# Kernel optimization log

Measured on AMD Instinct MI355X. Metric: run time of the kernel, lower is better.

The kernel has to match this reference:

```python
import jax, jax.numpy as jnp
import numpy as np
from jax import lax

ROWS, COLS, HID = 5, 5, 4
N = ROWS * COLS
NUM_NEURONS = 128


def _nbr_indices(i, direction):
    # Faithful to get_neighbor_hidden, including the row-wrap behavior of
    # 'col-1'/'col+1' (no column bounds check in the original code).
    row, col = divmod(i, COLS)
    up = (row - 1) * COLS + col
    dn = (row + 1) * COLS + col
    lf = row * COLS + col - 1
    rt = row * COLS + col + 1
    return [up, dn, lf, rt] if direction == 'f' else [up, dn, rt, lf]


def _gather_neighbors(h, idxs):
    # h: (N, bs, HID); returns (bs, 4) of the 4th hidden feature per neighbor
    bs = h.shape[1]
    cols_list = [h[j][:, 3] if 0 <= j < N else jnp.zeros((bs,), h.dtype) for j in idxs]
    return jnp.stack(cols_list, axis=1)


def _make_step(Wx, Wh, Wn, b, direction):
    # One timestep: nodes updated sequentially (node i sees already-updated
    # up/left neighbors within the same timestep, matching the torch loop).
    def step(carry, x_t):  # x_t: (N, bs)
        h, c = carry  # each (N, bs, HID)
        for i in range(N):
            nb = _gather_neighbors(h, _nbr_indices(i, direction))  # (bs,4)
            gates = x_t[i][:, None] @ Wx + h[i] @ Wh + nb @ Wn + b  # (bs,4H)
            ig, fg, og, cc = jnp.split(gates, 4, axis=1)
            nc = jax.nn.sigmoid(fg) * c[i] + jax.nn.sigmoid(ig) * jnp.tanh(cc)
            nh = jax.nn.sigmoid(og) * jnp.tanh(nc)
            h = h.at[i].set(nh)
            c = c.at[i].set(nc)
        return (h, c), None
    return step


def _forward(x, h0f, c0f, h0b, c0b, Wx_f, Wh_f, Wn_f, b_f,
             Wx_b, Wh_b, Wn_b, b_b, W_ff, b_ff, W_out, b_out):
    bs = x.shape[0]
    x_seq = jnp.transpose(x, (2, 1, 0))  # (T, N, bs)
    (hf, cf), _ = lax.scan(_make_step(Wx_f, Wh_f, Wn_f, b_f, 'f'), (h0f, c0f), x_seq)
    (hb, cb), _ = lax.scan(_make_step(Wx_b, Wh_b, Wn_b, b_b, 'b'), (h0b, c0b), x_seq[::-1])
    H_fwd = jnp.transpose(hf, (1, 0, 2))  # (bs, N, HID)
    H_bwd = jnp.transpose(hb, (1, 0, 2))
    H = jnp.concatenate([H_fwd, H_bwd], axis=2).reshape(bs, -1)  # (bs, 200)
    ff = jax.nn.sigmoid(H @ W_ff + b_ff)
    return jax.nn.softmax(ff @ W_out + b_out, axis=1)


def setup_inputs() -> dict:
    key = jax.random.key(0)
    ks = jax.random.split(key, 16)
    bs, T = 8192, 128
    d = {}
    d['x'] = jax.random.normal(ks[0], (bs, N, T), jnp.float32)
    for nm, k in zip(['h0f', 'c0f', 'h0b', 'c0b'], ks[1:5]):
        d[nm] = jax.random.normal(k, (N, bs, HID), jnp.float32) * 0.01
    def lin(k, i, o):
        return jax.random.normal(k, (i, o), jnp.float32) * (1.0 / np.sqrt(i))
    d['Wx_f'] = lin(ks[5], 1, 4 * HID)
    d['Wh_f'] = lin(ks[6], HID, 4 * HID)
    d['Wn_f'] = lin(ks[7], 4, 4 * HID)
    d['b_f'] = jnp.zeros((4 * HID,), jnp.float32)
    d['Wx_b'] = lin(ks[8], 1, 4 * HID)
    d['Wh_b'] = lin(ks[9], HID, 4 * HID)
    d['Wn_b'] = lin(ks[10], 4, 4 * HID)
    d['b_b'] = jnp.zeros((4 * HID,), jnp.float32)
    d['W_ff'] = lin(ks[11], N * 2 * HID, NUM_NEURONS)
    d['b_ff'] = jnp.zeros((NUM_NEURONS,), jnp.float32)
    d['W_out'] = lin(ks[12], NUM_NEURONS, 2)
    d['b_out'] = jnp.zeros((2,), jnp.float32)
    return d


def reference(x, h0f, c0f, h0b, c0b, Wx_f, Wh_f, Wn_f, b_f,
              Wx_b, Wh_b, Wn_b, b_b, W_ff, b_ff, W_out, b_out):
    return _forward(x, h0f, c0f, h0b, c0b, Wx_f, Wh_f, Wn_f, b_f,
                    Wx_b, Wh_b, Wn_b, b_b, W_ff, b_ff, W_out, b_out)
```

## Files before the change

kernel.cpp:

```cpp
#include <hip/hip_runtime.h>
#include <stddef.h>

#define BS 8192
#define NNODE 25
#define TT 128
#define TCH 16
#define NW (TT / TCH)
#define XPAD 65
#define LOG2E 1.4426950408889634f

typedef float v2f __attribute__((ext_vector_type(2)));
typedef float v4f __attribute__((ext_vector_type(4)));

__device__ __forceinline__ float ex2(float x) { return __builtin_amdgcn_exp2f(x); }
__device__ __forceinline__ float rcp_(float x) { return __builtin_amdgcn_rcpf(x); }

__device__ float g_hf[NNODE * BS * 4];
__device__ float g_hb[NNODE * BS * 4];

template <int K>
__device__ __forceinline__ float bcast4(float v) {
  int s = __builtin_bit_cast(int, v);
  int r = __builtin_amdgcn_update_dpp(0, s, (K * 0x55), 0xF, 0xF, true);
  return __builtin_bit_cast(float, r);
}

__device__ __forceinline__ void acc2(v2f& A, v2f& B, float s, v2f wa, v2f wb) {
  v2f sv = {s, s};
  A = __builtin_elementwise_fma(sv, wa, A);
  B = __builtin_elementwise_fma(sv, wb, B);
}

template <int DIR>
__device__ __forceinline__ void rnn_run(
    int tid, const float* __restrict__ xblk, float* __restrict__ xs,
    const float* __restrict__ h0, const float* __restrict__ c0,
    const float* __restrict__ Wx, const float* __restrict__ Wh,
    const float* __restrict__ Wn, const float* __restrict__ Bb,
    float* __restrict__ ho, int b) {
  const int d = tid & 3;
  const int bl = tid >> 2;
  const int cI = d, cF = 4 + d, cO = 8 + d, cC = 12 + d;
  const float sS = -LOG2E, sC = 2.0f * LOG2E;

  v2f wA[9], wB[9];
  wA[0] = v2f{sS * Wx[cI], sS * Wx[cF]};
  wB[0] = v2f{sS * Wx[cO], sC * Wx[cC]};
#pragma unroll
  for (int k = 0; k < 4; ++k) {
    wA[1 + k] = v2f{sS * Wh[k * 16 + cI], sS * Wh[k * 16 + cF]};
    wB[1 + k] = v2f{sS * Wh[k * 16 + cO], sC * Wh[k * 16 + cC]};
  }
  const int nrow[4] = {0, 1, DIR ? 3 : 2, DIR ? 2 : 3};
#pragma unroll
  for (int k = 0; k < 4; ++k) {
    wA[5 + k] = v2f{sS * Wn[nrow[k] * 16 + cI], sS * Wn[nrow[k] * 16 + cF]};
    wB[5 + k] = v2f{sS * Wn[nrow[k] * 16 + cO], sC * Wn[nrow[k] * 16 + cC]};
  }
  const v2f bA = {sS * Bb[cI], sS * Bb[cF]};
  const v2f bB = {sS * Bb[cO], sC * Bb[cC]};

  float h[NNODE], c[NNODE], b3[NNODE];
#pragma unroll
  for (int i = 0; i < NNODE; ++i) {
    h[i] = h0[(i * BS + b) * 4 + d];
    c[i] = c0[(i * BS + b) * 4 + d];
    b3[i] = bcast4<3>(h[i]);
  }

  const int t4 = tid & 3;
  const int s0 = tid >> 2;

  for (int w = 0; w < NW; ++w) {
    __syncthreads();
#pragma unroll
    for (int r = 0; r < NNODE; ++r) {
      const int seg = s0 + 64 * r;
      const int sbl = seg / 25;
      const int sii = seg - sbl * 25;
      const int tb = (DIR ? (TT - TCH - TCH * w) : (TCH * w)) + 4 * t4;
      const v4f v = *(const v4f*)(xblk + ((size_t)sbl * NNODE + sii) * TT + tb);
#pragma unroll
      for (int j = 0; j < 4; ++j) {
        const int kk = DIR ? (15 - 4 * t4 - j) : (4 * t4 + j);
        xs[(kk * NNODE + sii) * XPAD + sbl] = v[j];
      }
    }
    __syncthreads();

#pragma unroll 1
    for (int kk = 0; kk < TCH; ++kk) {
      float xq[NNODE];
#pragma unroll
      for (int i = 0; i < NNODE; ++i) xq[i] = xs[(kk * NNODE + i) * XPAD + bl];

#pragma unroll
      for (int r = 0; r < 5; ++r) {
        v2f PA[5], PB[5];
#pragma unroll
        for (int j = 0; j < 5; ++j) {
          const int i = r * 5 + j;
          const float f0 = bcast4<0>(h[i]);
          const float f1 = bcast4<1>(h[i]);
          const float f2 = bcast4<2>(h[i]);
          v2f A = bA, B = bB;
          acc2(A, B, xq[i], wA[0], wB[0]);
          acc2(A, B, f0, wA[1], wB[1]);
          acc2(A, B, f1, wA[2], wB[2]);
          acc2(A, B, f2, wA[3], wB[3]);
          acc2(A, B, b3[i], wA[4], wB[4]);
          if (i >= 5) acc2(A, B, b3[i - 5], wA[5], wB[5]);
          if (i < 20) acc2(A, B, b3[i + 5], wA[6], wB[6]);
          if (i < 24) acc2(A, B, b3[i + 1], wA[8], wB[8]);
          PA[j] = A;
          PB[j] = B;
        }

#pragma unroll
        for (int j = 0; j < 5; ++j) {
          const int i = r * 5 + j;
          v2f A = PA[j], B = PB[j];
          if (i >= 1) acc2(A, B, b3[i - 1], wA[7], wB[7]);

          const float Ei = ex2(A.x);
          const float Ef = ex2(A.y);
          const float Eo = ex2(B.x);
          const float Ec = ex2(B.y);
          const v2f Dif = v2f{Ei, Ef} + v2f{1.0f, 1.0f};
          const v2f Ecpm = v2f{Ec, Ec} + v2f{1.0f, -1.0f};
          const float P = Dif.x * Ecpm.x;
          const float num = fmaf(c[i], P, Ecpm.y * Dif.y);
          const float nc = num * rcp_(Dif.y * P);
          const float En = ex2(-2.0f * LOG2E * nc);
          const v2f Uno = v2f{En, Eo} + v2f{1.0f, 1.0f};
          const float hn = (1.0f - En) * rcp_(Uno.x * Uno.y);
          c[i] = nc;
          h[i] = hn;
          b3[i] = bcast4<3>(hn);
        }
      }
    }
  }

#pragma unroll
  for (int i = 0; i < NNODE; ++i) ho[(i * BS + b) * 4 + d] = h[i];
}

__global__ __launch_bounds__(256, 1) void rnn_kernel(
    const float* __restrict__ x,
    const float* __restrict__ h0f, const float* __restrict__ c0f,
    const float* __restrict__ h0b, const float* __restrict__ c0b,
    const float* __restrict__ Wxf, const float* __restrict__ Whf,
    const float* __restrict__ Wnf, const float* __restrict__ bf,
    const float* __restrict__ Wxb, const float* __restrict__ Whb,
    const float* __restrict__ Wnb, const float* __restrict__ bb_) {
  __shared__ float xs[TCH * NNODE * XPAD];
  const int tid = threadIdx.x;
  const int b = blockIdx.x * 64 + (tid >> 2);
  const float* xblk = x + (size_t)(blockIdx.x * 64) * (NNODE * TT);
  if (blockIdx.y == 0) {
    rnn_run<0>(tid, xblk, xs, h0f, c0f, Wxf, Whf, Wnf, bf, g_hf, b);
  } else {
    rnn_run<1>(tid, xblk, xs, h0b, c0b, Wxb, Whb, Wnb, bb_, g_hb, b);
  }
}

__global__ __launch_bounds__(256) void ff_kernel(
    const float* __restrict__ Wff, const float* __restrict__ bff,
    const float* __restrict__ Wout, const float* __restrict__ bout,
    float* __restrict__ out) {
  __shared__ float Hs[32][200];
  __shared__ float ffs[32][130];
  const int tid = threadIdx.x;
  const int b0 = blockIdx.x * 32;

  for (int idx = tid; idx < NNODE * 2 * 32; idx += 256) {
    const int i = idx >> 6;
    const int r = idx & 63;
    const int dir = r >> 5;
    const int bb = r & 31;
    const float* src = dir ? g_hb : g_hf;
    const v4f v = *(const v4f*)(src + ((size_t)(i * BS + b0 + bb)) * 4);
#pragma unroll
    for (int f = 0; f < 4; ++f) Hs[bb][i * 8 + dir * 4 + f] = v[f];
  }
  __syncthreads();

  {
    const int n = tid & 127;
    const int half = tid >> 7;
    float acc[16];
    const float bv = bff[n];
#pragma unroll
    for (int q = 0; q < 16; ++q) acc[q] = bv;
    for (int k = 0; k < 200; ++k) {
      const float w = Wff[k * 128 + n];
#pragma unroll
      for (int q = 0; q < 16; ++q)
        acc[q] = fmaf(Hs[half * 16 + q][k], w, acc[q]);
    }
#pragma unroll
    for (int q = 0; q < 16; ++q)
      ffs[half * 16 + q][n] = rcp_(1.0f + ex2(-LOG2E * acc[q]));
  }
  __syncthreads();

  if (tid < 64) {
    const int bb = tid >> 1;
    const int j = tid & 1;
    float z = bout[j];
    for (int n = 0; n < 128; ++n)
      z = fmaf(ffs[bb][n], Wout[n * 2 + j], z);
    const float zp = __shfl_xor(z, 1);
    const float m = fmaxf(z, zp);
    const float e = ex2(LOG2E * (z - m));
    const float ep = ex2(LOG2E * (zp - m));
    const float s = rcp_(e + ep);
    out[(size_t)(b0 + bb) * 2 + j] = e * s;
  }
}

extern "C" void kernel_launch(void* const* d_in, const int* in_sizes, int n_in,
                              void* d_out, int out_size, void* d_ws, size_t ws_size,
                              hipStream_t stream) {
  (void)in_sizes; (void)n_in; (void)out_size; (void)d_ws; (void)ws_size;
  const float* x    = (const float*)d_in[0];
  const float* h0f  = (const float*)d_in[1];
  const float* c0f  = (const float*)d_in[2];
  const float* h0b  = (const float*)d_in[3];
  const float* c0b  = (const float*)d_in[4];
  const float* Wxf  = (const float*)d_in[5];
  const float* Whf  = (const float*)d_in[6];
  const float* Wnf  = (const float*)d_in[7];
  const float* bf   = (const float*)d_in[8];
  const float* Wxb  = (const float*)d_in[9];
  const float* Whb  = (const float*)d_in[10];
  const float* Wnb  = (const float*)d_in[11];
  const float* bb   = (const float*)d_in[12];
  const float* Wff  = (const float*)d_in[13];
  const float* bff  = (const float*)d_in[14];
  const float* Wout = (const float*)d_in[15];
  const float* bout = (const float*)d_in[16];
  float* out = (float*)d_out;

  rnn_kernel<<<dim3(128, 2), dim3(256), 0, stream>>>(
      x, h0f, c0f, h0b, c0b, Wxf, Whf, Wnf, bf, Wxb, Whb, Wnb, bb);
  ff_kernel<<<dim3(256), dim3(256), 0, stream>>>(Wff, bff, Wout, bout, out);
}
```

Baseline: 569.5 us.

## Interleave two timesteps in a skewed wavefront to expose ILP in the node chain

The inner loop now handles two consecutive timesteps together. Node i of step k runs interleaved with node i-6 of step k+1, which is legal because the i-6 node's neighbours are already final for the right timestep. Sched barriers force an alternating X/Y instruction order so the two independent dependency chains overlap and hide transcendental and DPP latency. The cost is higher register pressure from the two x vectors and extra in-flight state, plus a more rigid schedule.

```diff
diff --git a/kernel.cpp b/kernel.cpp
--- a/kernel.cpp
+++ b/kernel.cpp
@@ -14,6 +14,7 @@
 
 __device__ __forceinline__ float ex2(float x) { return __builtin_amdgcn_exp2f(x); }
 __device__ __forceinline__ float rcp_(float x) { return __builtin_amdgcn_rcpf(x); }
+__device__ __forceinline__ void SB() { __builtin_amdgcn_sched_barrier(0); }
 
 __device__ float g_hf[NNODE * BS * 4];
 __device__ float g_hb[NNODE * BS * 4];
@@ -29,6 +30,45 @@
   v2f sv = {s, s};
   A = __builtin_elementwise_fma(sv, wa, A);
   B = __builtin_elementwise_fma(sv, wb, B);
+}
+
+__device__ __forceinline__ void gates(
+    int i, float x, const float* __restrict__ h, const float* __restrict__ b3,
+    const v2f* __restrict__ wA, const v2f* __restrict__ wB, v2f bA, v2f bB,
+    v2f& A, v2f& B) {
+  const float f0 = bcast4<0>(h[i]);
+  const float f1 = bcast4<1>(h[i]);
+  const float f2 = bcast4<2>(h[i]);
+  A = bA; B = bB;
+  acc2(A, B, x, wA[0], wB[0]);
+  acc2(A, B, f0, wA[1], wB[1]);
+  acc2(A, B, f1, wA[2], wB[2]);
+  acc2(A, B, f2, wA[3], wB[3]);
+  acc2(A, B, b3[i], wA[4], wB[4]);
+  if (i >= 5) acc2(A, B, b3[i - 5], wA[5], wB[5]);
+  if (i < 20) acc2(A, B, b3[i + 5], wA[6], wB[6]);
+  if (i >= 1) acc2(A, B, b3[i - 1], wA[7], wB[7]);
+  if (i < 24) acc2(A, B, b3[i + 1], wA[8], wB[8]);
+}
+
+__device__ __forceinline__ void node_full(
+    int i, float x, float* __restrict__ h, float* __restrict__ c,
+    float* __restrict__ b3, const v2f* __restrict__ wA,
+    const v2f* __restrict__ wB, v2f bA, v2f bB) {
+  v2f A, B;
+  gates(i, x, h, b3, wA, wB, bA, bB, A, B);
+  const float Ei = ex2(A.x), Ef = ex2(A.y), Eo = ex2(B.x), Ec = ex2(B.y);
+  const v2f Dif = v2f{Ei, Ef} + v2f{1.0f, 1.0f};
+  const v2f Ecp = v2f{Ec, Ec} + v2f{1.0f, -1.0f};
+  const float P = Dif.x * Ecp.x;
+  const float num = fmaf(c[i], P, Ecp.y * Dif.y);
+  const float nc = num * rcp_(Dif.y * P);
+  const float En = ex2(-2.0f * LOG2E * nc);
+  const v2f Uno = v2f{En, Eo} + v2f{1.0f, 1.0f};
+  const float hn = (1.0f - En) * rcp_(Uno.x * Uno.y);
+  c[i] = nc;
+  h[i] = hn;
+  b3[i] = bcast4<3>(hn);
 }
 
 template <int DIR>
@@ -89,56 +129,71 @@
     __syncthreads();
 
 #pragma unroll 1
-    for (int kk = 0; kk < TCH; ++kk) {
-      float xq[NNODE];
-#pragma unroll
-      for (int i = 0; i < NNODE; ++i) xq[i] = xs[(kk * NNODE + i) * XPAD + bl];
-
-#pragma unroll
-      for (int r = 0; r < 5; ++r) {
-        v2f PA[5], PB[5];
-#pragma unroll
-        for (int j = 0; j < 5; ++j) {
-          const int i = r * 5 + j;
-          const float f0 = bcast4<0>(h[i]);
-          const float f1 = bcast4<1>(h[i]);
-          const float f2 = bcast4<2>(h[i]);
-          v2f A = bA, B = bB;
-          acc2(A, B, xq[i], wA[0], wB[0]);
-          acc2(A, B, f0, wA[1], wB[1]);
-          acc2(A, B, f1, wA[2], wB[2]);
-          acc2(A, B, f2, wA[3], wB[3]);
-          acc2(A, B, b3[i], wA[4], wB[4]);
-          if (i >= 5) acc2(A, B, b3[i - 5], wA[5], wB[5]);
-          if (i < 20) acc2(A, B, b3[i + 5], wA[6], wB[6]);
-          if (i < 24) acc2(A, B, b3[i + 1], wA[8], wB[8]);
-          PA[j] = A;
-          PB[j] = B;
-        }
-
-#pragma unroll
-        for (int j = 0; j < 5; ++j) {
-          const int i = r * 5 + j;
-          v2f A = PA[j], B = PB[j];
-          if (i >= 1) acc2(A, B, b3[i - 1], wA[7], wB[7]);
-
-          const float Ei = ex2(A.x);
-          const float Ef = ex2(A.y);
-          const float Eo = ex2(B.x);
-          const float Ec = ex2(B.y);
-          const v2f Dif = v2f{Ei, Ef} + v2f{1.0f, 1.0f};
-          const v2f Ecpm = v2f{Ec, Ec} + v2f{1.0f, -1.0f};
-          const float P = Dif.x * Ecpm.x;
-          const float num = fmaf(c[i], P, Ecpm.y * Dif.y);
-          const float nc = num * rcp_(Dif.y * P);
-          const float En = ex2(-2.0f * LOG2E * nc);
-          const v2f Uno = v2f{En, Eo} + v2f{1.0f, 1.0f};
-          const float hn = (1.0f - En) * rcp_(Uno.x * Uno.y);
-          c[i] = nc;
-          h[i] = hn;
-          b3[i] = bcast4<3>(hn);
-        }
+    for (int kp = 0; kp < TCH / 2; ++kp) {
+      const int k0 = 2 * kp, k1 = 2 * kp + 1;
+      float xq0[NNODE], xq1[NNODE];
+#pragma unroll
+      for (int i = 0; i < NNODE; ++i) {
+        xq0[i] = xs[(k0 * NNODE + i) * XPAD + bl];
+        xq1[i] = xs[(k1 * NNODE + i) * XPAD + bl];
       }
+
+#pragma unroll
+      for (int i = 0; i < 6; ++i)
+        node_full(i, xq0[i], h, c, b3, wA, wB, bA, bB);
+
+#pragma unroll
+      for (int m = 0; m < 19; ++m) {
+        const int iX = 6 + m;
+        const int iY = m;
+        v2f XA, XB;
+        gates(iX, xq0[iX], h, b3, wA, wB, bA, bB, XA, XB);
+        const float Eix = ex2(XA.x), Efx = ex2(XA.y);
+        const float Eox = ex2(XB.x), Ecx = ex2(XB.y);
+        SB();
+        v2f YA, YB;
+        gates(iY, xq1[iY], h, b3, wA, wB, bA, bB, YA, YB);
+        const float Eiy = ex2(YA.x), Efy = ex2(YA.y);
+        const float Eoy = ex2(YB.x), Ecy = ex2(YB.y);
+        SB();
+        const v2f DifX = v2f{Eix, Efx} + v2f{1.0f, 1.0f};
+        const v2f EcpX = v2f{Ecx, Ecx} + v2f{1.0f, -1.0f};
+        const float PX = DifX.x * EcpX.x;
+        const float numX = fmaf(c[iX], PX, EcpX.y * DifX.y);
+        const float r1X = rcp_(DifX.y * PX);
+        SB();
+        const v2f DifY = v2f{Eiy, Efy} + v2f{1.0f, 1.0f};
+        const v2f EcpY = v2f{Ecy, Ecy} + v2f{1.0f, -1.0f};
+        const float PY = DifY.x * EcpY.x;
+        const float numY = fmaf(c[iY], PY, EcpY.y * DifY.y);
+        const float r1Y = rcp_(DifY.y * PY);
+        SB();
+        const float ncX = numX * r1X;
+        c[iX] = ncX;
+        const float EnX = ex2(-2.0f * LOG2E * ncX);
+        SB();
+        const float ncY = numY * r1Y;
+        c[iY] = ncY;
+        const float EnY = ex2(-2.0f * LOG2E * ncY);
+        SB();
+        const v2f UnoX = v2f{EnX, Eox} + v2f{1.0f, 1.0f};
+        const float r2X = rcp_(UnoX.x * UnoX.y);
+        SB();
+        const v2f UnoY = v2f{EnY, Eoy} + v2f{1.0f, 1.0f};
+        const float r2Y = rcp_(UnoY.x * UnoY.y);
+        SB();
+        const float hnX = (1.0f - EnX) * r2X;
+        h[iX] = hnX;
+        b3[iX] = bcast4<3>(hnX);
+        const float hnY = (1.0f - EnY) * r2Y;
+        h[iY] = hnY;
+        b3[iY] = bcast4<3>(hnY);
+        SB();
+      }
+
+#pragma unroll
+      for (int i = 19; i < 25; ++i)
+        node_full(i, xq1[i], h, c, b3, wA, wB, bA, bB);
     }
   }
 
```

After: 563.2 us. About the same (-1.1%).
